# Optimization experiments

Measured on AMD Instinct MI355X. Metric: run time of the kernel, lower is better.

The kernel has to match this reference:

```python
import jax, jax.numpy as jnp
import numpy as np

N_ENTS = 50000
N_EDGES = 500000
N_RELS = 200
RANK = 128
N_LAYERS = 2
RRELU_SLOPE = (1.0 / 8.0 + 1.0 / 3.0) / 2.0  # F.rrelu eval-mode: mean of default lower/upper


def setup_inputs() -> dict:
    key = jax.random.key(0)
    ks = jax.random.split(key, 9)
    return {
        "ent_emb": jax.random.normal(ks[0], (N_ENTS, RANK), dtype=jnp.float32),
        "rel_emb": jax.random.normal(ks[1], (N_RELS, RANK), dtype=jnp.float32),
        "norm": jax.random.uniform(ks[2], (N_ENTS, 1), dtype=jnp.float32),
        "Wn": jax.random.normal(ks[3], (N_LAYERS, RANK, RANK), dtype=jnp.float32) * 0.05,
        "Wl": jax.random.normal(ks[4], (N_LAYERS, RANK, RANK), dtype=jnp.float32) * 0.05,
        "Wa": jax.random.normal(ks[5], (N_LAYERS, RANK, RANK), dtype=jnp.float32) * 0.05,
        "src": jax.random.randint(ks[6], (N_EDGES,), 0, N_ENTS, dtype=jnp.int32),
        "dst": jax.random.randint(ks[7], (N_EDGES,), 0, N_ENTS, dtype=jnp.int32),
        "etype": jax.random.randint(ks[8], (N_EDGES,), 0, N_RELS, dtype=jnp.int32),
    }


def reference(ent_emb, rel_emb, norm, Wn, Wl, Wa, src, dst, etype):
    n = ent_emb.shape[0]
    # in-degree mask (same graph across layers)
    in_deg = jax.ops.segment_sum(jnp.ones_like(dst, dtype=jnp.float32), dst, num_segments=n)
    has_in = (in_deg > 0)[:, None]  # [N,1]
    h = ent_emb
    for l in range(Wn.shape[0]):
        # edge gather + add + linear: msg = (h[src] + rel_emb[etype]) @ Wn[l]
        msg = (h[src] + rel_emb[etype]) @ Wn[l]  # [E, rank]
        # scatter-sum into destination nodes, then per-node norm
        agg = jax.ops.segment_sum(msg, dst, num_segments=n) * norm  # [N, rank]
        # masked self-loop: loop_weight where in_degree>0, else alone_loop_weight
        loop = jnp.where(has_in, h @ Wl[l], h @ Wa[l])
        h = agg + loop
        # rrelu in eval mode == leaky relu with slope (1/8 + 1/3)/2
        h = jnp.where(h >= 0, h, h * RRELU_SLOPE)
        # dropout=0.0 -> identity
    return h
```

## Files before the change

kernel.cpp:

```cpp
#include <hip/hip_runtime.h>

#define SLOPE 0.22916666666666666f
#define ALONE_CAP 2048

typedef __attribute__((ext_vector_type(8))) short bfrag;
typedef __attribute__((ext_vector_type(4))) float ffrag;

__device__ __forceinline__ unsigned short rne16(float f) {
    unsigned u = __float_as_uint(f);
    return (unsigned short)((u + 0x7FFFu + ((u >> 16) & 1u)) >> 16);
}
__device__ __forceinline__ float bf2f(unsigned short h) {
    return __uint_as_float(((unsigned)h) << 16);
}
__device__ __forceinline__ unsigned packsplit(float f) {
    unsigned short hi = rne16(f);
    unsigned short lo = rne16(f - bf2f(hi));
    return ((unsigned)hi << 16) | lo;
}
__device__ __forceinline__ float recon(unsigned u) {
    return __uint_as_float(u & 0xFFFF0000u) + __uint_as_float(u << 16);
}
__device__ __forceinline__ float4 recon4(uint4 u) {
    return make_float4(recon(u.x), recon(u.y), recon(u.z), recon(u.w));
}

__global__ __launch_bounds__(256) void prep_kernel(
    const int* __restrict__ dst, int* __restrict__ deg, int e, int eb,
    const float* __restrict__ ent, unsigned* __restrict__ Esp,
    int total4, int cb,
    const float* __restrict__ Wn, const float* __restrict__ Wl,
    ushort* __restrict__ packW) {
    int b = blockIdx.x;
    if (b < eb) {
        int i = b * 256 + threadIdx.x;
        if (i < e) atomicAdd(&deg[dst[i]], 1);
    } else if (b < eb + cb) {
        int i = (b - eb) * 256 + threadIdx.x;
        if (i >= total4) return;
        float4 v = ((const float4*)ent)[i];
        uint4 w;
        w.x = packsplit(v.x); w.y = packsplit(v.y);
        w.z = packsplit(v.z); w.w = packsplit(v.w);
        ((uint4*)Esp)[i] = w;
    } else {
        int t = (b - eb - cb) * 256 + threadIdx.x;
        if (t >= 4 * 4 * 128 * 4) return;
        int quad = t & 3;
        int nn   = (t >> 2) & 127;
        int kc   = (t >> 9) & 3;
        int mat  = t >> 11;
        const float* W = ((mat & 1) ? Wl : Wn) + (mat >> 1) * 16384;
        ushort* oh = packW + mat * 32768;
        ushort* ol = oh + 16384;
        int obase = ((kc * 128 + nn) * 4 + quad) * 8;
        #pragma unroll
        for (int j = 0; j < 8; ++j) {
            float w = W[(kc * 32 + quad * 8 + j) * 128 + nn];
            unsigned short hi = rne16(w);
            oh[obase + j] = hi;
            ol[obase + j] = rne16(w - bf2f(hi));
        }
    }
}

__global__ __launch_bounds__(256) void scan_kernel(const int* __restrict__ deg,
                                                   int* __restrict__ partial,
                                                   int* __restrict__ flag,
                                                   int* __restrict__ row_off,
                                                   int* __restrict__ alone_list,
                                                   int* __restrict__ alone_count, int n) {
    __shared__ int wsum[4];
    __shared__ int sbase;
    int bid = blockIdx.x;
    int t = threadIdx.x, lane = t & 63, wid = t >> 6;
    int base = bid * 1024;
    int i0 = base + t * 4;
    int v0 = (i0 + 0 < n) ? deg[i0 + 0] : 0;
    int v1 = (i0 + 1 < n) ? deg[i0 + 1] : 0;
    int v2 = (i0 + 2 < n) ? deg[i0 + 2] : 0;
    int v3 = (i0 + 3 < n) ? deg[i0 + 3] : 0;
    int s = v0 + v1 + v2 + v3;
    int x = s;
    #pragma unroll
    for (int off = 1; off < 64; off <<= 1) {
        int y = __shfl_up(x, off, 64);
        if (lane >= off) x += y;
    }
    if (lane == 63) wsum[wid] = x;
    __syncthreads();
    if (t == 0) {
        int total = wsum[0] + wsum[1] + wsum[2] + wsum[3];
        __hip_atomic_store(&partial[bid], total, __ATOMIC_RELEASE, __HIP_MEMORY_SCOPE_AGENT);
        __hip_atomic_store(&flag[bid], 1, __ATOMIC_RELEASE, __HIP_MEMORY_SCOPE_AGENT);
    }
    if (wid == 0) {
        int v = 0;
        if (lane < bid) {
            while (__hip_atomic_load(&flag[lane], __ATOMIC_ACQUIRE, __HIP_MEMORY_SCOPE_AGENT) == 0) {}
            v = __hip_atomic_load(&partial[lane], __ATOMIC_ACQUIRE, __HIP_MEMORY_SCOPE_AGENT);
        }
        #pragma unroll
        for (int off = 1; off < 64; off <<= 1) v += __shfl_xor(v, off, 64);
        if (lane == 0) sbase = v;
    }
    __syncthreads();
    int wbase = 0;
    #pragma unroll
    for (int w = 0; w < 4; ++w) { int ws = wsum[w]; if (w < wid) wbase += ws; }
    int p = sbase + wbase + x - s;
    if (i0 + 0 <= n) row_off[i0 + 0] = p;
    p += v0;
    if (i0 + 1 <= n) row_off[i0 + 1] = p;
    p += v1;
    if (i0 + 2 <= n) row_off[i0 + 2] = p;
    p += v2;
    if (i0 + 3 <= n) row_off[i0 + 3] = p;
    if (i0 + 0 < n && v0 == 0) { int q = atomicAdd(alone_count, 1); if (q < ALONE_CAP) alone_list[q] = i0; }
    if (i0 + 1 < n && v1 == 0) { int q = atomicAdd(alone_count, 1); if (q < ALONE_CAP) alone_list[q] = i0 + 1; }
    if (i0 + 2 < n && v2 == 0) { int q = atomicAdd(alone_count, 1); if (q < ALONE_CAP) alone_list[q] = i0 + 2; }
    if (i0 + 3 < n && v3 == 0) { int q = atomicAdd(alone_count, 1); if (q < ALONE_CAP) alone_list[q] = i0 + 3; }
}

__global__ __launch_bounds__(256) void scatter_kernel(
    const int* __restrict__ src, const int* __restrict__ dst,
    const int* __restrict__ ety, const int* __restrict__ row_off,
    int* __restrict__ cursor, unsigned* __restrict__ edges, int e) {
    int i = blockIdx.x * 256 + threadIdx.x;
    if (i < e) {
        int v = dst[i];
        int pos = row_off[v] + atomicAdd(&cursor[v], 1);
        edges[pos] = (unsigned)src[i] | ((unsigned)ety[i] << 16);
    }
}

template <int SPLIT>
__global__ __launch_bounds__(256) void agg_kernel(
    const float* __restrict__ hf, const unsigned* __restrict__ hs,
    const float* __restrict__ rel,
    const float* __restrict__ norm, const int* __restrict__ row_off,
    const unsigned* __restrict__ edges, unsigned* __restrict__ Ssp, int n) {
    __shared__ float part[2][128];
    int wv = threadIdx.x >> 6, lane = threadIdx.x & 63;
    int slot = wv >> 1, w = wv & 1;
    int v = blockIdx.x * 2 + slot;
    bool active = v < n;
    int s0 = 0, s1 = 0;
    if (active) { s0 = row_off[v]; s1 = row_off[v + 1]; }
    int mid = (s0 + s1 + 1) >> 1;
    int b0 = w ? mid : s0;
    int b1 = w ? s1 : mid;
    int half = lane >> 5;
    int c4 = (lane & 31) * 4;
    float4 acc = make_float4(0.f, 0.f, 0.f, 0.f);
    int e = b0;
    for (; e + 3 < b1; e += 4) {
        unsigned q0 = edges[e + half];
        unsigned q1 = edges[e + 2 + half];
        float4 h0, h1;
        if (SPLIT) {
            h0 = recon4(*(const uint4*)&hs[(size_t)(q0 & 0xFFFFu) * 128 + c4]);
            h1 = recon4(*(const uint4*)&hs[(size_t)(q1 & 0xFFFFu) * 128 + c4]);
        } else {
            h0 = *(const float4*)&hf[(size_t)(q0 & 0xFFFFu) * 128 + c4];
            h1 = *(const float4*)&hf[(size_t)(q1 & 0xFFFFu) * 128 + c4];
        }
        float4 r0 = *(const float4*)&rel[(size_t)(q0 >> 16) * 128 + c4];
        float4 r1 = *(const float4*)&rel[(size_t)(q1 >> 16) * 128 + c4];
        acc.x += (h0.x + r0.x) + (h1.x + r1.x);
        acc.y += (h0.y + r0.y) + (h1.y + r1.y);
        acc.z += (h0.z + r0.z) + (h1.z + r1.z);
        acc.w += (h0.w + r0.w) + (h1.w + r1.w);
    }
    for (; e + 1 < b1; e += 2) {
        unsigned q0 = edges[e + half];
        float4 h0 = SPLIT ? recon4(*(const uint4*)&hs[(size_t)(q0 & 0xFFFFu) * 128 + c4])
                          : *(const float4*)&hf[(size_t)(q0 & 0xFFFFu) * 128 + c4];
        float4 r0 = *(const float4*)&rel[(size_t)(q0 >> 16) * 128 + c4];
        acc.x += h0.x + r0.x; acc.y += h0.y + r0.y;
        acc.z += h0.z + r0.z; acc.w += h0.w + r0.w;
    }
    if (e < b1 && half == 0) {
        unsigned q0 = edges[e];
        float4 h0 = SPLIT ? recon4(*(const uint4*)&hs[(size_t)(q0 & 0xFFFFu) * 128 + c4])
                          : *(const float4*)&hf[(size_t)(q0 & 0xFFFFu) * 128 + c4];
        float4 r0 = *(const float4*)&rel[(size_t)(q0 >> 16) * 128 + c4];
        acc.x += h0.x + r0.x; acc.y += h0.y + r0.y;
        acc.z += h0.z + r0.z; acc.w += h0.w + r0.w;
    }
    acc.x += __shfl_xor(acc.x, 32, 64);
    acc.y += __shfl_xor(acc.y, 32, 64);
    acc.z += __shfl_xor(acc.z, 32, 64);
    acc.w += __shfl_xor(acc.w, 32, 64);
    if (active && w == 0 && half == 0) *(float4*)&part[slot][c4] = acc;
    __syncthreads();
    if (active && w == 1 && half == 0) {
        float4 p = *(const float4*)&part[slot][c4];
        float nm = norm[v];
        uint4 o;
        o.x = packsplit((acc.x + p.x) * nm);
        o.y = packsplit((acc.y + p.y) * nm);
        o.z = packsplit((acc.z + p.z) * nm);
        o.w = packsplit((acc.w + p.w) * nm);
        *(uint4*)&Ssp[(size_t)v * 128 + c4] = o;
    }
}

__global__ __launch_bounds__(128) void gemm_mfma_kernel(
    const unsigned* __restrict__ Ssp, const unsigned* Hsp,
    const ushort* __restrict__ Pnh, const ushort* __restrict__ Pnl,
    const ushort* __restrict__ Plh, const ushort* __restrict__ Pll,
    float* __restrict__ out, unsigned* Osp, int n) {
    const int tid = threadIdx.x;
    const int wave = tid >> 6, lane = tid & 63;
    const int quad = lane >> 4, l16 = lane & 15;
    const int row_base = blockIdx.x * 64 + wave * 32;

    int r0c = row_base + l16;       if (r0c > n - 1) r0c = n - 1;
    int r1c = row_base + 16 + l16;  if (r1c > n - 1) r1c = n - 1;

    ffrag acc[2][8];
    #pragma unroll
    for (int rt = 0; rt < 2; ++rt)
        #pragma unroll
        for (int ct = 0; ct < 8; ++ct) acc[rt][ct] = (ffrag)0.f;

    #pragma unroll 1
    for (int half = 0; half < 2; ++half) {
        const unsigned* A = half ? Hsp : Ssp;
        const ushort* Pbh = half ? Plh : Pnh;
        const ushort* Pbl = half ? Pll : Pnl;
        #pragma unroll 1
        for (int kc = 0; kc < 4; ++kc) {
            const int koff = kc * 32 + quad * 8;
            uint4 a0a = *(const uint4*)(A + (size_t)r0c * 128 + koff);
            uint4 a0b = *(const uint4*)(A + (size_t)r0c * 128 + koff + 4);
            uint4 a1a = *(const uint4*)(A + (size_t)r1c * 128 + koff);
            uint4 a1b = *(const uint4*)(A + (size_t)r1c * 128 + koff + 4);
            bfrag ah[2], al[2];
            #pragma unroll
            for (int j = 0; j < 4; ++j) {
                unsigned u0 = ((const unsigned*)&a0a)[j];
                unsigned u1 = ((const unsigned*)&a0b)[j];
                ah[0][j]     = (short)(u0 >> 16); al[0][j]     = (short)(u0 & 0xFFFFu);
                ah[0][j + 4] = (short)(u1 >> 16); al[0][j + 4] = (short)(u1 & 0xFFFFu);
                unsigned u2 = ((const unsigned*)&a1a)[j];
                unsigned u3 = ((const unsigned*)&a1b)[j];
                ah[1][j]     = (short)(u2 >> 16); al[1][j]     = (short)(u2 & 0xFFFFu);
                ah[1][j + 4] = (short)(u3 >> 16); al[1][j + 4] = (short)(u3 & 0xFFFFu);
            }
            bfrag bh[8], bl[8];
            #pragma unroll
            for (int ct = 0; ct < 8; ++ct) {
                int bidx = ((kc * 128 + ct * 16 + l16) * 4 + quad) * 8;
                bh[ct] = *(const bfrag*)(Pbh + bidx);
                bl[ct] = *(const bfrag*)(Pbl + bidx);
            }
            #pragma unroll
            for (int rt = 0; rt < 2; ++rt)
                #pragma unroll
                for (int ct = 0; ct < 8; ++ct)
                    acc[rt][ct] = __builtin_amdgcn_mfma_f32_16x16x32_bf16(
                        ah[rt], bh[ct], acc[rt][ct], 0, 0, 0);
            #pragma unroll
            for (int rt = 0; rt < 2; ++rt)
                #pragma unroll
                for (int ct = 0; ct < 8; ++ct)
                    acc[rt][ct] = __builtin_amdgcn_mfma_f32_16x16x32_bf16(
                        ah[rt], bl[ct], acc[rt][ct], 0, 0, 0);
            #pragma unroll
            for (int rt = 0; rt < 2; ++rt)
                #pragma unroll
                for (int ct = 0; ct < 8; ++ct)
                    acc[rt][ct] = __builtin_amdgcn_mfma_f32_16x16x32_bf16(
                        al[rt], bh[ct], acc[rt][ct], 0, 0, 0);
        }
    }

    __syncthreads();

    #pragma unroll
    for (int rt = 0; rt < 2; ++rt) {
        #pragma unroll
        for (int ct = 0; ct < 8; ++ct) {
            #pragma unroll
            for (int rg = 0; rg < 4; ++rg) {
                int r = row_base + rt * 16 + quad * 4 + rg;
                if (r < n) {
                    int c = ct * 16 + l16;
                    float v = acc[rt][ct][rg];
                    v = v >= 0.f ? v : v * SLOPE;
                    if (out) out[(size_t)r * 128 + c] = v;
                    if (Osp) Osp[(size_t)r * 128 + c] = packsplit(v);
                }
            }
        }
    }
}

__global__ __launch_bounds__(128) void fixup_kernel(
    const float* __restrict__ Hrows, int by_node,
    const float* __restrict__ Wa,
    const int* __restrict__ alone_list, const int* __restrict__ alone_count,
    float* out, unsigned* Osp, float* asave) {
    int cnt = *alone_count;
    if (cnt > ALONE_CAP) cnt = ALONE_CAP;
    int t = threadIdx.x;
    for (int i = blockIdx.x; i < cnt; i += gridDim.x) {
        int v = alone_list[i];
        const float* hrow = Hrows + (size_t)(by_node ? v : i) * 128;
        float acc = 0.f;
        for (int k = 0; k < 128; ++k)
            acc += hrow[k] * Wa[k * 128 + t];
        float o = acc >= 0.f ? acc : acc * SLOPE;
        if (out) out[(size_t)v * 128 + t] = o;
        if (Osp) Osp[(size_t)v * 128 + t] = packsplit(o);
        if (asave) asave[(size_t)i * 128 + t] = o;
    }
}

extern "C" void kernel_launch(void* const* d_in, const int* in_sizes, int n_in,
                              void* d_out, int out_size, void* d_ws, size_t ws_size,
                              hipStream_t stream) {
    const float* ent  = (const float*)d_in[0];
    const float* rel  = (const float*)d_in[1];
    const float* norm = (const float*)d_in[2];
    const float* Wn   = (const float*)d_in[3];
    const float* Wl   = (const float*)d_in[4];
    const float* Wa   = (const float*)d_in[5];
    const int*   src  = (const int*)d_in[6];
    const int*   dst  = (const int*)d_in[7];
    const int*   ety  = (const int*)d_in[8];
    float* out = (float*)d_out;

    const int n = in_sizes[2];
    const int e = in_sizes[7];

    char* ws = (char*)d_ws;
    int* deg         = (int*)ws;
    int* cursor      = deg + n;
    int* alone_count = cursor + n;
    int* partial     = alone_count + 1;
    int* flags       = partial + 64;
    size_t zbytes = (size_t)(2 * n + 1 + 128) * sizeof(int);
    size_t p = (zbytes + 255) & ~(size_t)255;
    int* row_off = (int*)(ws + p);
    p += (((size_t)(n + 1) * 4) + 255) & ~(size_t)255;
    int* alone_list = (int*)(ws + p);
    p += (((size_t)ALONE_CAP * 4) + 255) & ~(size_t)255;
    float* asave = (float*)(ws + p);
    p += (((size_t)ALONE_CAP * 128 * 4) + 255) & ~(size_t)255;
    unsigned* edges = (unsigned*)(ws + p);
    p += (((size_t)e * 4) + 255) & ~(size_t)255;
    unsigned* Ssp = (unsigned*)(ws + p);
    p += (((size_t)n * 128 * 4) + 255) & ~(size_t)255;
    unsigned* Esp = (unsigned*)(ws + p);
    p += (((size_t)n * 128 * 4) + 255) & ~(size_t)255;
    ushort* packW = (ushort*)(ws + p);
    p += 4 * 32768 * 2;

    const int eb = (e + 255) / 256;
    const int cb = (n * 32 + 255) / 256;
    const int nparts = (n + 1023) / 1024;
    const int gb = (n + 63) / 64;
    const int ab = (n + 1) / 2;

    hipMemsetAsync(ws, 0, zbytes, stream);
    prep_kernel<<<eb + cb + 32, 256, 0, stream>>>(dst, deg, e, eb,
                                                  ent, Esp, n * 32, cb,
                                                  Wn, Wl, packW);
    scan_kernel<<<nparts, 256, 0, stream>>>(deg, partial, flags, row_off,
                                            alone_list, alone_count, n);
    scatter_kernel<<<eb, 256, 0, stream>>>(src, dst, ety, row_off, cursor, edges, e);

    agg_kernel<0><<<ab, 256, 0, stream>>>(ent, nullptr, rel, norm, row_off, edges, Ssp, n);
    gemm_mfma_kernel<<<gb, 128, 0, stream>>>(Ssp, Esp,
                                             packW, packW + 16384,
                                             packW + 32768, packW + 49152,
                                             nullptr, Esp, n);
    fixup_kernel<<<16, 128, 0, stream>>>(ent, 1, Wa, alone_list, alone_count,
                                         nullptr, Esp, asave);

    agg_kernel<1><<<ab, 256, 0, stream>>>(nullptr, Esp, rel, norm, row_off, edges, Ssp, n);
    gemm_mfma_kernel<<<gb, 128, 0, stream>>>(Ssp, Esp,
                                             packW + 65536, packW + 81920,
                                             packW + 98304, packW + 114688,
                                             out, nullptr, n);
    fixup_kernel<<<16, 128, 0, stream>>>(asave, 0, Wa + 16384, alone_list, alone_count,
                                         out, nullptr, nullptr);
}
```

Measured before the change: 308.1 us.

## Fuse edge aggregation and MFMA GEMM into a single per-layer kernel

```diff
diff --git a/kernel.cpp b/kernel.cpp
--- a/kernel.cpp
+++ b/kernel.cpp
@@ -135,164 +135,141 @@
 }
 
 template <int SPLIT>
-__global__ __launch_bounds__(256) void agg_kernel(
-    const float* __restrict__ hf, const unsigned* __restrict__ hs,
-    const float* __restrict__ rel,
-    const float* __restrict__ norm, const int* __restrict__ row_off,
-    const unsigned* __restrict__ edges, unsigned* __restrict__ Ssp, int n) {
-    __shared__ float part[2][128];
-    int wv = threadIdx.x >> 6, lane = threadIdx.x & 63;
-    int slot = wv >> 1, w = wv & 1;
-    int v = blockIdx.x * 2 + slot;
-    bool active = v < n;
-    int s0 = 0, s1 = 0;
-    if (active) { s0 = row_off[v]; s1 = row_off[v + 1]; }
-    int mid = (s0 + s1 + 1) >> 1;
-    int b0 = w ? mid : s0;
-    int b1 = w ? s1 : mid;
-    int half = lane >> 5;
-    int c4 = (lane & 31) * 4;
-    float4 acc = make_float4(0.f, 0.f, 0.f, 0.f);
-    int e = b0;
-    for (; e + 3 < b1; e += 4) {
-        unsigned q0 = edges[e + half];
-        unsigned q1 = edges[e + 2 + half];
-        float4 h0, h1;
-        if (SPLIT) {
-            h0 = recon4(*(const uint4*)&hs[(size_t)(q0 & 0xFFFFu) * 128 + c4]);
-            h1 = recon4(*(const uint4*)&hs[(size_t)(q1 & 0xFFFFu) * 128 + c4]);
-        } else {
-            h0 = *(const float4*)&hf[(size_t)(q0 & 0xFFFFu) * 128 + c4];
-            h1 = *(const float4*)&hf[(size_t)(q1 & 0xFFFFu) * 128 + c4];
-        }
-        float4 r0 = *(const float4*)&rel[(size_t)(q0 >> 16) * 128 + c4];
-        float4 r1 = *(const float4*)&rel[(size_t)(q1 >> 16) * 128 + c4];
-        acc.x += (h0.x + r0.x) + (h1.x + r1.x);
-        acc.y += (h0.y + r0.y) + (h1.y + r1.y);
-        acc.z += (h0.z + r0.z) + (h1.z + r1.z);
-        acc.w += (h0.w + r0.w) + (h1.w + r1.w);
-    }
-    for (; e + 1 < b1; e += 2) {
-        unsigned q0 = edges[e + half];
-        float4 h0 = SPLIT ? recon4(*(const uint4*)&hs[(size_t)(q0 & 0xFFFFu) * 128 + c4])
-                          : *(const float4*)&hf[(size_t)(q0 & 0xFFFFu) * 128 + c4];
-        float4 r0 = *(const float4*)&rel[(size_t)(q0 >> 16) * 128 + c4];
-        acc.x += h0.x + r0.x; acc.y += h0.y + r0.y;
-        acc.z += h0.z + r0.z; acc.w += h0.w + r0.w;
-    }
-    if (e < b1 && half == 0) {
-        unsigned q0 = edges[e];
-        float4 h0 = SPLIT ? recon4(*(const uint4*)&hs[(size_t)(q0 & 0xFFFFu) * 128 + c4])
-                          : *(const float4*)&hf[(size_t)(q0 & 0xFFFFu) * 128 + c4];
-        float4 r0 = *(const float4*)&rel[(size_t)(q0 >> 16) * 128 + c4];
-        acc.x += h0.x + r0.x; acc.y += h0.y + r0.y;
-        acc.z += h0.z + r0.z; acc.w += h0.w + r0.w;
-    }
-    acc.x += __shfl_xor(acc.x, 32, 64);
-    acc.y += __shfl_xor(acc.y, 32, 64);
-    acc.z += __shfl_xor(acc.z, 32, 64);
-    acc.w += __shfl_xor(acc.w, 32, 64);
-    if (active && w == 0 && half == 0) *(float4*)&part[slot][c4] = acc;
-    __syncthreads();
-    if (active && w == 1 && half == 0) {
-        float4 p = *(const float4*)&part[slot][c4];
-        float nm = norm[v];
-        uint4 o;
-        o.x = packsplit((acc.x + p.x) * nm);
-        o.y = packsplit((acc.y + p.y) * nm);
-        o.z = packsplit((acc.z + p.z) * nm);
-        o.w = packsplit((acc.w + p.w) * nm);
-        *(uint4*)&Ssp[(size_t)v * 128 + c4] = o;
-    }
-}
-
-__global__ __launch_bounds__(128) void gemm_mfma_kernel(
-    const unsigned* __restrict__ Ssp, const unsigned* Hsp,
+__global__ __launch_bounds__(256) void layer_kernel(
+    const float* __restrict__ gf, const unsigned* __restrict__ gs,
+    const float* __restrict__ rel, const float* __restrict__ norm,
+    const int* __restrict__ row_off, const unsigned* __restrict__ edges,
+    const unsigned* __restrict__ Hsp,
     const ushort* __restrict__ Pnh, const ushort* __restrict__ Pnl,
     const ushort* __restrict__ Plh, const ushort* __restrict__ Pll,
-    float* __restrict__ out, unsigned* Osp, int n) {
+    float* __restrict__ out, unsigned* __restrict__ Osp, int n) {
+    __shared__ float S[64][132];
     const int tid = threadIdx.x;
     const int wave = tid >> 6, lane = tid & 63;
+    const int half = lane >> 5;
+    const int c4 = (lane & 31) * 4;
+    const int row0 = blockIdx.x * 64;
+
+    for (int i = 0; i < 16; ++i) {
+        const int lrow = wave * 16 + i;
+        const int v = row0 + lrow;
+        float4 acc = make_float4(0.f, 0.f, 0.f, 0.f);
+        float nm = 0.f;
+        if (v < n) {
+            nm = norm[v];
+            int s0 = row_off[v], s1 = row_off[v + 1];
+            int e = s0;
+            for (; e + 3 < s1; e += 4) {
+                unsigned q0 = edges[e + half];
+                unsigned q1 = edges[e + 2 + half];
+                float4 h0, h1;
+                if (SPLIT) {
+                    h0 = recon4(*(const uint4*)&gs[(size_t)(q0 & 0xFFFFu) * 128 + c4]);
+                    h1 = recon4(*(const uint4*)&gs[(size_t)(q1 & 0xFFFFu) * 128 + c4]);
+                } else {
+                    h0 = *(const float4*)&gf[(size_t)(q0 & 0xFFFFu) * 128 + c4];
+                    h1 = *(const float4*)&gf[(size_t)(q1 & 0xFFFFu) * 128 + c4];
+                }
+                float4 r0 = *(const float4*)&rel[(size_t)(q0 >> 16) * 128 + c4];
+                float4 r1 = *(const float4*)&rel[(size_t)(q1 >> 16) * 128 + c4];
+                acc.x += (h0.x + r0.x) + (h1.x + r1.x);
+                acc.y += (h0.y + r0.y) + (h1.y + r1.y);
+                acc.z += (h0.z + r0.z) + (h1.z + r1.z);
+                acc.w += (h0.w + r0.w) + (h1.w + r1.w);
+            }
+            for (; e + 1 < s1; e += 2) {
+                unsigned q0 = edges[e + half];
+                float4 h0 = SPLIT ? recon4(*(const uint4*)&gs[(size_t)(q0 & 0xFFFFu) * 128 + c4])
+                                  : *(const float4*)&gf[(size_t)(q0 & 0xFFFFu) * 128 + c4];
+                float4 r0 = *(const float4*)&rel[(size_t)(q0 >> 16) * 128 + c4];
+                acc.x += h0.x + r0.x; acc.y += h0.y + r0.y;
+                acc.z += h0.z + r0.z; acc.w += h0.w + r0.w;
+            }
+            if (e < s1 && half == 0) {
+                unsigned q0 = edges[e];
+                float4 h0 = SPLIT ? recon4(*(const uint4*)&gs[(size_t)(q0 & 0xFFFFu) * 128 + c4])
+                                  : *(const float4*)&gf[(size_t)(q0 & 0xFFFFu) * 128 + c4];
+                float4 r0 = *(const float4*)&rel[(size_t)(q0 >> 16) * 128 + c4];
+                acc.x += h0.x + r0.x; acc.y += h0.y + r0.y;
+                acc.z += h0.z + r0.z; acc.w += h0.w + r0.w;
+            }
+        }
+        acc.x += __shfl_xor(acc.x, 32, 64);
+        acc.y += __shfl_xor(acc.y, 32, 64);
+        acc.z += __shfl_xor(acc.z, 32, 64);
+        acc.w += __shfl_xor(acc.w, 32, 64);
+        if (half == 0)
+            *(float4*)&S[lrow][c4] = make_float4(acc.x * nm, acc.y * nm,
+                                                 acc.z * nm, acc.w * nm);
+    }
+    __syncthreads();
+
     const int quad = lane >> 4, l16 = lane & 15;
-    const int row_base = blockIdx.x * 64 + wave * 32;
-
-    int r0c = row_base + l16;       if (r0c > n - 1) r0c = n - 1;
-    int r1c = row_base + 16 + l16;  if (r1c > n - 1) r1c = n - 1;
-
-    ffrag acc[2][8];
+    const int lr = wave * 16 + l16;
+    int rc = row0 + lr; if (rc > n - 1) rc = n - 1;
+
+    ffrag acc[8];
     #pragma unroll
-    for (int rt = 0; rt < 2; ++rt)
-        #pragma unroll
-        for (int ct = 0; ct < 8; ++ct) acc[rt][ct] = (ffrag)0.f;
+    for (int ct = 0; ct < 8; ++ct) acc[ct] = (ffrag)0.f;
 
     #pragma unroll 1
-    for (int half = 0; half < 2; ++half) {
-        const unsigned* A = half ? Hsp : Ssp;
-        const ushort* Pbh = half ? Plh : Pnh;
-        const ushort* Pbl = half ? Pll : Pnl;
-        #pragma unroll 1
-        for (int kc = 0; kc < 4; ++kc) {
-            const int koff = kc * 32 + quad * 8;
-            uint4 a0a = *(const uint4*)(A + (size_t)r0c * 128 + koff);
-            uint4 a0b = *(const uint4*)(A + (size_t)r0c * 128 + koff + 4);
-            uint4 a1a = *(const uint4*)(A + (size_t)r1c * 128 + koff);
-            uint4 a1b = *(const uint4*)(A + (size_t)r1c * 128 + koff + 4);
-            bfrag ah[2], al[2];
-            #pragma unroll
-            for (int j = 0; j < 4; ++j) {
-                unsigned u0 = ((const unsigned*)&a0a)[j];
-                unsigned u1 = ((const unsigned*)&a0b)[j];
-                ah[0][j]     = (short)(u0 >> 16); al[0][j]     = (short)(u0 & 0xFFFFu);
-                ah[0][j + 4] = (short)(u1 >> 16); al[0][j + 4] = (short)(u1 & 0xFFFFu);
-                unsigned u2 = ((const unsigned*)&a1a)[j];
-                unsigned u3 = ((const unsigned*)&a1b)[j];
-                ah[1][j]     = (short)(u2 >> 16); al[1][j]     = (short)(u2 & 0xFFFFu);
-                ah[1][j + 4] = (short)(u3 >> 16); al[1][j + 4] = (short)(u3 & 0xFFFFu);
-            }
-            bfrag bh[8], bl[8];
-            #pragma unroll
-            for (int ct = 0; ct < 8; ++ct) {
-                int bidx = ((kc * 128 + ct * 16 + l16) * 4 + quad) * 8;
-                bh[ct] = *(const bfrag*)(Pbh + bidx);
-                bl[ct] = *(const bfrag*)(Pbl + bidx);
-            }
-            #pragma unroll
-            for (int rt = 0; rt < 2; ++rt)
-                #pragma unroll
-                for (int ct = 0; ct < 8; ++ct)
-                    acc[rt][ct] = __builtin_amdgcn_mfma_f32_16x16x32_bf16(
-                        ah[rt], bh[ct], acc[rt][ct], 0, 0, 0);
-            #pragma unroll
-            for (int rt = 0; rt < 2; ++rt)
-                #pragma unroll
-                for (int ct = 0; ct < 8; ++ct)
-                    acc[rt][ct] = __builtin_amdgcn_mfma_f32_16x16x32_bf16(
-                        ah[rt], bl[ct], acc[rt][ct], 0, 0, 0);
-            #pragma unroll
-            for (int rt = 0; rt < 2; ++rt)
-                #pragma unroll
-                for (int ct = 0; ct < 8; ++ct)
-                    acc[rt][ct] = __builtin_amdgcn_mfma_f32_16x16x32_bf16(
-                        al[rt], bh[ct], acc[rt][ct], 0, 0, 0);
-        }
-    }
-
-    __syncthreads();
+    for (int kc = 0; kc < 4; ++kc) {
+        const int koff = kc * 32 + quad * 8;
+        float4 sa = *(const float4*)&S[lr][koff];
+        float4 sb = *(const float4*)&S[lr][koff + 4];
+        float sv[8] = {sa.x, sa.y, sa.z, sa.w, sb.x, sb.y, sb.z, sb.w};
+        bfrag ah, al;
+        #pragma unroll
+        for (int j = 0; j < 8; ++j) {
+            unsigned short hi = rne16(sv[j]);
+            ah[j] = (short)hi;
+            al[j] = (short)rne16(sv[j] - bf2f(hi));
+        }
+        #pragma unroll
+        for (int ct = 0; ct < 8; ++ct) {
+            int bidx = ((kc * 128 + ct * 16 + l16) * 4 + quad) * 8;
+            bfrag bh = *(const bfrag*)(Pnh + bidx);
+            bfrag bl = *(const bfrag*)(Pnl + bidx);
+            acc[ct] = __builtin_amdgcn_mfma_f32_16x16x32_bf16(ah, bh, acc[ct], 0, 0, 0);
+            acc[ct] = __builtin_amdgcn_mfma_f32_16x16x32_bf16(ah, bl, acc[ct], 0, 0, 0);
+            acc[ct] = __builtin_amdgcn_mfma_f32_16x16x32_bf16(al, bh, acc[ct], 0, 0, 0);
+        }
+    }
+    #pragma unroll 1
+    for (int kc = 0; kc < 4; ++kc) {
+        const int koff = kc * 32 + quad * 8;
+        uint4 ua = *(const uint4*)(Hsp + (size_t)rc * 128 + koff);
+        uint4 ub = *(const uint4*)(Hsp + (size_t)rc * 128 + koff + 4);
+        bfrag ah, al;
+        #pragma unroll
+        for (int j = 0; j < 4; ++j) {
+            unsigned u0 = ((const unsigned*)&ua)[j];
+            unsigned u1 = ((const unsigned*)&ub)[j];
+            ah[j]     = (short)(u0 >> 16); al[j]     = (short)(u0 & 0xFFFFu);
+            ah[j + 4] = (short)(u1 >> 16); al[j + 4] = (short)(u1 & 0xFFFFu);
+        }
+        #pragma unroll
+        for (int ct = 0; ct < 8; ++ct) {
+            int bidx = ((kc * 128 + ct * 16 + l16) * 4 + quad) * 8;
+            bfrag bh = *(const bfrag*)(Plh + bidx);
+            bfrag bl = *(const bfrag*)(Pll + bidx);
+            acc[ct] = __builtin_amdgcn_mfma_f32_16x16x32_bf16(ah, bh, acc[ct], 0, 0, 0);
+            acc[ct] = __builtin_amdgcn_mfma_f32_16x16x32_bf16(ah, bl, acc[ct], 0, 0, 0);
+            acc[ct] = __builtin_amdgcn_mfma_f32_16x16x32_bf16(al, bh, acc[ct], 0, 0, 0);
+        }
+    }
 
     #pragma unroll
-    for (int rt = 0; rt < 2; ++rt) {
-        #pragma unroll
-        for (int ct = 0; ct < 8; ++ct) {
-            #pragma unroll
-            for (int rg = 0; rg < 4; ++rg) {
-                int r = row_base + rt * 16 + quad * 4 + rg;
-                if (r < n) {
-                    int c = ct * 16 + l16;
-                    float v = acc[rt][ct][rg];
-                    v = v >= 0.f ? v : v * SLOPE;
-                    if (out) out[(size_t)r * 128 + c] = v;
-                    if (Osp) Osp[(size_t)r * 128 + c] = packsplit(v);
-                }
+    for (int ct = 0; ct < 8; ++ct) {
+        #pragma unroll
+        for (int rg = 0; rg < 4; ++rg) {
+            int r = row0 + wave * 16 + quad * 4 + rg;
+            if (r < n) {
+                int c = ct * 16 + l16;
+                float v = acc[ct][rg];
+                v = v >= 0.f ? v : v * SLOPE;
+                if (out) out[(size_t)r * 128 + c] = v;
+                if (Osp) Osp[(size_t)r * 128 + c] = packsplit(v);
             }
         }
     }
@@ -352,9 +329,9 @@
     p += (((size_t)ALONE_CAP * 128 * 4) + 255) & ~(size_t)255;
     unsigned* edges = (unsigned*)(ws + p);
     p += (((size_t)e * 4) + 255) & ~(size_t)255;
-    unsigned* Ssp = (unsigned*)(ws + p);
+    unsigned* Esp = (unsigned*)(ws + p);
     p += (((size_t)n * 128 * 4) + 255) & ~(size_t)255;
-    unsigned* Esp = (unsigned*)(ws + p);
+    unsigned* H1sp = (unsigned*)(ws + p);
     p += (((size_t)n * 128 * 4) + 255) & ~(size_t)255;
     ushort* packW = (ushort*)(ws + p);
     p += 4 * 32768 * 2;
@@ -363,7 +340,6 @@
     const int cb = (n * 32 + 255) / 256;
     const int nparts = (n + 1023) / 1024;
     const int gb = (n + 63) / 64;
-    const int ab = (n + 1) / 2;
 
     hipMemsetAsync(ws, 0, zbytes, stream);
     prep_kernel<<<eb + cb + 32, 256, 0, stream>>>(dst, deg, e, eb,
@@ -373,19 +349,19 @@
                                             alone_list, alone_count, n);
     scatter_kernel<<<eb, 256, 0, stream>>>(src, dst, ety, row_off, cursor, edges, e);
 
-    agg_kernel<0><<<ab, 256, 0, stream>>>(ent, nullptr, rel, norm, row_off, edges, Ssp, n);
-    gemm_mfma_kernel<<<gb, 128, 0, stream>>>(Ssp, Esp,
-                                             packW, packW + 16384,
-                                             packW + 32768, packW + 49152,
-                                             nullptr, Esp, n);
+    layer_kernel<0><<<gb, 256, 0, stream>>>(ent, nullptr, rel, norm, row_off, edges,
+                                            Esp,
+                                            packW, packW + 16384,
+                                            packW + 32768, packW + 49152,
+                                            nullptr, H1sp, n);
     fixup_kernel<<<16, 128, 0, stream>>>(ent, 1, Wa, alone_list, alone_count,
-                                         nullptr, Esp, asave);
-
-    agg_kernel<1><<<ab, 256, 0, stream>>>(nullptr, Esp, rel, norm, row_off, edges, Ssp, n);
-    gemm_mfma_kernel<<<gb, 128, 0, stream>>>(Ssp, Esp,
-                                             packW + 65536, packW + 81920,
-                                             packW + 98304, packW + 114688,
-                                             out, nullptr, n);
+                                         nullptr, H1sp, asave);
+
+    layer_kernel<1><<<gb, 256, 0, stream>>>(nullptr, H1sp, rel, norm, row_off, edges,
+                                            H1sp,
+                                            packW + 65536, packW + 81920,
+                                            packW + 98304, packW + 114688,
+                                            out, nullptr, n);
     fixup_kernel<<<16, 128, 0, stream>>>(asave, 0, Wa + 16384, alone_list, alone_count,
                                          out, nullptr, nullptr);
 }
```

Result: slower. 327.0 us (+6.2%).
